# Optimization experiments

Measured on AMD Instinct MI355X. Metric: run time of the kernel, lower is better.

Reference implementation:

```python
import jax, jax.numpy as jnp
import numpy as np

N_LOC, N_EVT, E = 100000, 200000, 1000000
F_LOC, F_EVT, H = 128, 128, 64


def setup_inputs() -> dict:
    key = jax.random.key(0)
    ks = jax.random.split(key, 12)
    s = lambda k, shp: jax.random.normal(k, shp, dtype=jnp.float32) * (1.0 / np.sqrt(shp[0]))
    return {
        "loc_x": jax.random.normal(ks[0], (N_LOC, F_LOC), dtype=jnp.float32),
        "evt_x": jax.random.normal(ks[1], (N_EVT, F_EVT), dtype=jnp.float32),
        "edge_index": jax.random.randint(ks[2], (2, E), 0, N_LOC, dtype=jnp.int64),
        # projections (stored as (in, out))
        "W_loc": s(ks[3], (F_LOC, H)), "b_loc": jnp.zeros((H,), jnp.float32),
        "W_evt": s(ks[4], (F_EVT, H)), "b_evt": jnp.zeros((H,), jnp.float32),
        # SAGEConv: lin_l (on aggregated src, with bias), lin_r (on dst root, no bias)
        "W_l": s(ks[5], (H, H)), "b_l": jnp.zeros((H,), jnp.float32),
        "W_r": s(ks[6], (H, H)),
        # head MLP
        "W_h1": s(ks[7], (H, H // 2)), "b_h1": jnp.zeros((H // 2,), jnp.float32),
        "W_h2": s(ks[8], (H // 2, 1)), "b_h2": jnp.zeros((1,), jnp.float32),
    }


def reference(loc_x, evt_x, edge_index, W_loc, b_loc, W_evt, b_evt,
              W_l, b_l, W_r, W_h1, b_h1, W_h2, b_h2):
    # node projections + ReLU
    loc_h = jax.nn.relu(loc_x @ W_loc + b_loc)   # [N_loc, H]
    evt_h = jax.nn.relu(evt_x @ W_evt + b_evt)   # [N_evt, H]

    src, dst = edge_index[0], edge_index[1]      # event -> location
    n_loc = loc_h.shape[0]
    # mean aggregation of source (event) features onto destination (location) nodes
    msg_sum = jax.ops.segment_sum(evt_h[src], dst, num_segments=n_loc)   # [N_loc, H]
    cnt = jax.ops.segment_sum(jnp.ones_like(dst, dtype=loc_h.dtype), dst,
                              num_segments=n_loc)
    agg = msg_sum / jnp.maximum(cnt, 1.0)[:, None]
    # SAGEConv: lin_l(agg) + lin_r(root), then ReLU
    loc_h = jax.nn.relu(agg @ W_l + b_l + loc_h @ W_r)

    # prediction head
    h = jax.nn.relu(loc_h @ W_h1 + b_h1)
    logits = (h @ W_h2 + b_h2)[:, 0]             # [N_loc]
    return logits
```

## Files before the change

### kernel.cpp

```cpp
#include <hip/hip_runtime.h>


#define N_LOC 100000
#define N_EVT 200000
#define E_CNT 1000000
#define NTILES 6250
#define NBKT   256
#define BKT_L  391
#define CAPG   6000
#define QCAP   32
#define BKT_BLK 512
#define PERB   1954

#define PROJ_EVT_BLK 1536
#define PROJ_LOC_BLK 768
#define PROJ_BLK_TOT (PROJ_EVT_BLK + PROJ_LOC_BLK)
#define EVT_TILES 12500
#define LOC_TILES 6250
#define HEAD_BLK  1024

typedef __attribute__((ext_vector_type(8))) short short8;
typedef __attribute__((ext_vector_type(4))) float floatx4;
typedef __attribute__((ext_vector_type(8))) unsigned short ushort8v;

__device__ __forceinline__ float b2f(unsigned short u) {
    unsigned int x = ((unsigned int)u) << 16;
    return __builtin_bit_cast(float, x);
}
__device__ __forceinline__ unsigned short f2b(float f) {
    unsigned int x = __builtin_bit_cast(unsigned int, f);
    unsigned int r = (x + 0x7fffu + ((x >> 16) & 1u)) >> 16;
    return (unsigned short)r;
}
__device__ __forceinline__ float loadf(const void* p, int f32, size_t i) {
    return f32 ? ((const float*)p)[i] : b2f(((const unsigned short*)p)[i]);
}

__global__ __launch_bounds__(256) void prep_kernel(
    const void* t0, const void* t1, const int* eidx,
    const void* t3, const void* t4, const void* t5, const void* t6,
    const void* t7, const void* t8, const void* t9, const void* t10,
    const void* t11, const void* t12, const void* t13,
    int* flags, int* gbc, unsigned short* __restrict__ wp_all) {
    int b = blockIdx.x, tid = threadIdx.x;
    __shared__ int s0, s1;

    if (b == 14) { gbc[tid] = 0; return; }

    if (b >= 15) {
        int pb = b - 15;
        const void* W; int K, N, bstart, off;
        if (pb < 4)       { W = t5;  K = 128; N = 64; bstart = 0;  off = 0; }
        else if (pb < 8)  { W = t3;  K = 128; N = 64; bstart = 4;  off = 8192; }
        else if (pb < 10) { W = t7;  K = 64;  N = 64; bstart = 8;  off = 16384; }
        else if (pb < 12) { W = t9;  K = 64;  N = 64; bstart = 10; off = 20480; }
        else              { W = t10; K = 64;  N = 32; bstart = 12; off = 24576; }
        if (tid == 0) s0 = 0;
        __syncthreads();
        int nsamp = 2 * K * N; if (nsamp > 1024) nsamp = 1024;
        const unsigned short* h = (const unsigned short*)W;
        int susp = 0;
        for (int i = tid; i < nsamp; i += 256)
            if (((h[i] >> 7) & 0xFF) >= 0x90) susp++;
        if (susp) atomicAdd(&s0, susp);
        __syncthreads();
        int f32 = (s0 * 16 >= nsamp) ? 1 : 0;

        int idx  = (pb - bstart) * 256 + tid;
        int nk   = K >> 5;
        int f    = idx >> 6;
        int lane = idx & 63;
        int t  = f / nk;
        int kk = f - t * nk;
        int n  = t * 16 + (lane & 15);
        int k0 = kk * 32 + (lane >> 4) * 8;
        unsigned short tmp[8];
#pragma unroll
        for (int j = 0; j < 8; ++j) {
            size_t src = (size_t)(k0 + j) * N + n;
            tmp[j] = f32 ? f2b(((const float*)W)[src])
                         : ((const unsigned short*)W)[src];
        }
#pragma unroll
        for (int j = 0; j < 8; ++j) wp_all[(size_t)off + (size_t)idx * 8 + j] = tmp[j];
        return;
    }

    if (tid == 0) { s0 = 0; s1 = 0; }
    __syncthreads();
    if (b == 13) {
        if (tid < 128) {
            if (eidx[2 * tid] != 0) atomicAdd(&s0, 1);
            if (eidx[2 * tid + 1] != 0) atomicAdd(&s1, 1);
        }
        __syncthreads();
        if (tid == 0) flags[2] = (s1 == 0 && s0 > 32) ? 1 : 0;
        return;
    }
    const void* ptrs[13] = {t0, t1, t3, t4, t5, t6, t7, t8, t9, t10, t11, t12, t13};
    const int   cnts[13] = {12800000, 25600000, 8192, 64, 8192, 64,
                            4096, 64, 4096, 2048, 32, 32, 1};
    const int   slot[13] = {0, 1, 3, 4, 5, 6, 7, 8, 9, 10, 11, 12, 13};
    int nsamp = 2 * cnts[b];
    if (nsamp > 1024) nsamp = 1024;
    const unsigned short* h = (const unsigned short*)ptrs[b];
    int susp = 0;
    for (int i = tid; i < nsamp; i += 256)
        if (((h[i] >> 7) & 0xFF) >= 0x90) susp++;
    if (susp) atomicAdd(&s0, susp);
    __syncthreads();
    if (tid == 0) flags[slot[b]] = (s0 * 16 >= nsamp) ? 1 : 0;
}

__global__ __launch_bounds__(256, 3) void proj_both_kernel(
    const void* __restrict__ evt_x, const void* __restrict__ loc_x,
    const unsigned short* __restrict__ wp_all,
    const void* __restrict__ b_evt, const void* __restrict__ b_loc,
    unsigned short* __restrict__ evt_h, unsigned short* __restrict__ loc_h,
    const int* __restrict__ flags) {
    __shared__ unsigned short bs[8192];
    int blk = blockIdx.x;
    int tid = threadIdx.x, lane = tid & 63, wv = tid >> 6;
    int l15 = lane & 15, quad = lane >> 4;

    const void* X; const unsigned short* Wp; const void* bias;
    unsigned short* Y; int fx, fb, w0, nw, ntile;
    if (blk < PROJ_EVT_BLK) {
        X = evt_x; Wp = wp_all;        bias = b_evt; Y = evt_h;
        fx = flags[1]; fb = flags[6];
        w0 = blk * 4 + wv; nw = PROJ_EVT_BLK * 4; ntile = EVT_TILES;
    } else {
        X = loc_x; Wp = wp_all + 8192; bias = b_loc; Y = loc_h;
        fx = flags[0]; fb = flags[4];
        w0 = (blk - PROJ_EVT_BLK) * 4 + wv; nw = PROJ_LOC_BLK * 4; ntile = LOC_TILES;
    }

    {
        const short8* src = reinterpret_cast<const short8*>(Wp);
        short8* dst = reinterpret_cast<short8*>(bs);
#pragma unroll
        for (int i = 0; i < 4; ++i) dst[tid + i * 256] = src[tid + i * 256];
    }
    __syncthreads();

    float bv[4];
#pragma unroll
    for (int q = 0; q < 4; ++q) bv[q] = loadf(bias, fb, q * 16 + l15);

    if (w0 >= ntile) return;

    auto mfma_store = [&](const short8* a, int t) {
        floatx4 acc[4];
#pragma unroll
        for (int q = 0; q < 4; ++q) acc[q] = (floatx4)0.0f;
#pragma unroll
        for (int q = 0; q < 4; ++q) {
            short8 bq[4];
#pragma unroll
            for (int kk = 0; kk < 4; ++kk)
                bq[kk] = *reinterpret_cast<const short8*>(
                    &bs[((q * 4 + kk) * 64 + lane) * 8]);
#pragma unroll
            for (int kk = 0; kk < 4; ++kk)
                acc[q] = __builtin_amdgcn_mfma_f32_16x16x32_bf16(
                    a[kk], bq[kk], acc[q], 0, 0, 0);
        }
#pragma unroll
        for (int q = 0; q < 4; ++q)
#pragma unroll
            for (int r = 0; r < 4; ++r) {
                float v = acc[q][r] + bv[q];
                v = v > 0.0f ? v : 0.0f;
                Y[(size_t)(t * 16 + quad * 4 + r) * 64 + q * 16 + l15] = f2b(v);
            }
    };

    if (fx) {
        const float* Xf = (const float*)X;
        float4 pf[8];
        auto issueF = [&](int t) {
            const float* xr = Xf + (size_t)(t * 16 + l15) * 128 + quad * 8;
#pragma unroll
            for (int kk = 0; kk < 4; ++kk) {
                pf[kk * 2]     = *reinterpret_cast<const float4*>(xr + kk * 32);
                pf[kk * 2 + 1] = *reinterpret_cast<const float4*>(xr + kk * 32 + 4);
            }
        };
        issueF(w0);
        for (int t = w0; t < ntile; t += nw) {
            short8 a[4];
#pragma unroll
            for (int kk = 0; kk < 4; ++kk) {
                float4 p0 = pf[kk * 2], p1 = pf[kk * 2 + 1];
                short8 v;
                v[0] = (short)f2b(p0.x); v[1] = (short)f2b(p0.y);
                v[2] = (short)f2b(p0.z); v[3] = (short)f2b(p0.w);
                v[4] = (short)f2b(p1.x); v[5] = (short)f2b(p1.y);
                v[6] = (short)f2b(p1.z); v[7] = (short)f2b(p1.w);
                a[kk] = v;
            }
            int tn = t + nw;
            if (tn < ntile) issueF(tn);
            mfma_store(a, t);
        }
    } else {
        const unsigned short* Xh = (const unsigned short*)X;
        short8 an[4];
        auto issueH = [&](int t) {
            const unsigned short* xr = Xh + (size_t)(t * 16 + l15) * 128 + quad * 8;
#pragma unroll
            for (int kk = 0; kk < 4; ++kk)
                an[kk] = *reinterpret_cast<const short8*>(xr + kk * 32);
        };
        issueH(w0);
        for (int t = w0; t < ntile; t += nw) {
            short8 a[4];
#pragma unroll
            for (int kk = 0; kk < 4; ++kk) a[kk] = an[kk];
            int tn = t + nw;
            if (tn < ntile) issueH(tn);
            mfma_store(a, t);
        }
    }
}

__global__ __launch_bounds__(256) void bucket_kernel(
    const int* __restrict__ eidx, uint2* __restrict__ bkt,
    int* __restrict__ gbc, const int* __restrict__ flags) {
    __shared__ uint2 queue[NBKT][QCAP];
    __shared__ int qcnt[NBKT];
    int tid = threadIdx.x, blk = blockIdx.x;
    qcnt[tid] = 0;
    __syncthreads();
    int f64 = flags[2];
    const long long* e64 = (const long long*)eidx;
    int e0 = blk * PERB;
    int e1 = e0 + PERB; if (e1 > E_CNT) e1 = E_CNT;
    const int rounds = (PERB + 255) / 256;

    for (int r = 0; r < rounds; ++r) {
        int e = e0 + r * 256 + tid;
        if (e < e1) {
            int src, dst;
            if (f64) { src = (int)e64[e]; dst = (int)e64[E_CNT + e]; }
            else     { src = eidx[e];     dst = eidx[E_CNT + e]; }
            if ((unsigned)dst < (unsigned)N_LOC && (unsigned)src < (unsigned)N_EVT) {
                int bk = dst / BKT_L;
                int pos = atomicAdd(&qcnt[bk], 1);
                if (pos < QCAP) {
                    queue[bk][pos] = make_uint2((unsigned)src, (unsigned)dst);
                } else {
                    int p = atomicAdd(&gbc[bk], 1);
                    if (p < CAPG) bkt[(size_t)bk * CAPG + p] = make_uint2(src, dst);
                }
            }
        }
        __syncthreads();
        int n = qcnt[tid]; if (n > QCAP) n = QCAP;
        while (n >= 16) {
            int gp = atomicAdd(&gbc[tid], 16);
            if (gp + 16 <= CAPG) {
                uint2* d = bkt + (size_t)tid * CAPG + gp;
#pragma unroll
                for (int j = 0; j < 16; ++j) d[j] = queue[tid][j];
            }
#pragma unroll
            for (int j = 16; j < QCAP; ++j) queue[tid][j - 16] = queue[tid][j];
            n -= 16;
        }
        qcnt[tid] = n;
        __syncthreads();
    }
    int n = qcnt[tid]; if (n > QCAP) n = QCAP;
    if (n > 0) {
        int gp = atomicAdd(&gbc[tid], n);
        for (int j = 0; j < n; ++j)
            if (gp + j < CAPG) bkt[(size_t)tid * CAPG + gp + j] = queue[tid][j];
    }
}

__global__ __launch_bounds__(256) void csr_build_kernel(
    const uint2* __restrict__ bkt, const int* __restrict__ gbc,
    int* __restrict__ rowptr, int* __restrict__ csr) {
    __shared__ int sg[256];
    __shared__ int lcnt[512];
    __shared__ int lscan[512];
    __shared__ int lcsr[CAPG];
    int b = blockIdx.x, tid = threadIdx.x;
    int loc0 = b * BKT_L;
    int nloc = N_LOC - loc0; if (nloc > BKT_L) nloc = BKT_L;

    int gv = gbc[tid]; if (gv > CAPG) gv = CAPG;
    sg[tid] = gv;
    __syncthreads();
    for (int d = 1; d < 256; d <<= 1) {
        int x = (tid >= d) ? sg[tid - d] : 0;
        __syncthreads();
        sg[tid] += x;
        __syncthreads();
    }
    int cntE = gbc[b]; if (cntE > CAPG) cntE = CAPG;
    int base = sg[b] - cntE;
    const uint2* bp = bkt + (size_t)b * CAPG;

    int i0 = tid, i1 = tid + 256;
    lcnt[i0] = 0; lcnt[i1] = 0;
    __syncthreads();
    for (int i = tid; i < cntE; i += 256) {
        int d = (int)bp[i].y - loc0;
        atomicAdd(&lcnt[d], 1);
    }
    __syncthreads();
    lscan[i0] = lcnt[i0]; lscan[i1] = lcnt[i1];
    __syncthreads();
    for (int d = 1; d < 512; d <<= 1) {
        int v0 = (i0 >= d) ? lscan[i0 - d] : 0;
        int v1 = (i1 >= d) ? lscan[i1 - d] : 0;
        __syncthreads();
        lscan[i0] += v0; lscan[i1] += v1;
        __syncthreads();
    }
    for (int i = tid; i < nloc; i += 256) {
        int excl = lscan[i] - lcnt[i];
        rowptr[loc0 + i] = base + excl;
        lcnt[i] = excl;
    }
    if (b == NBKT - 1 && tid == 0) rowptr[N_LOC] = base + cntE;
    __syncthreads();
    for (int i = tid; i < cntE; i += 256) {
        uint2 pr = bp[i];
        int d = (int)pr.y - loc0;
        int p = atomicAdd(&lcnt[d], 1);
        if (p < CAPG) lcsr[p] = (int)pr.x;
    }
    __syncthreads();
    for (int i = tid; i < cntE; i += 256) csr[base + i] = lcsr[i];
}

__global__ __launch_bounds__(256) void aggregate_kernel(
    const unsigned short* __restrict__ evt_h,
    const int* __restrict__ rowptr, const int* __restrict__ csr,
    unsigned short* __restrict__ agg, int N) {
    int wid  = (blockIdx.x * 256 + threadIdx.x) >> 6;
    int lane = threadIdx.x & 63;
    int eo = lane >> 3, cg = lane & 7;
    if (wid >= N) return;
    int e0 = rowptr[wid], e1 = rowptr[wid + 1];
    float a[8];
#pragma unroll
    for (int k = 0; k < 8; ++k) a[k] = 0.0f;

    int j = e0;
    for (; j + 16 <= e1; j += 16) {
        int s0 = csr[j + eo];
        int s1 = csr[j + 8 + eo];
        ushort8v v0 = *reinterpret_cast<const ushort8v*>(
            evt_h + (size_t)s0 * 64 + cg * 8);
        ushort8v v1 = *reinterpret_cast<const ushort8v*>(
            evt_h + (size_t)s1 * 64 + cg * 8);
#pragma unroll
        for (int k = 0; k < 8; ++k) a[k] += b2f(v0[k]) + b2f(v1[k]);
    }
    for (; j < e1; j += 8) {
        int jj = j + eo;
        bool c = jj < e1;
        int s = csr[c ? jj : j];
        ushort8v v = *reinterpret_cast<const ushort8v*>(
            evt_h + (size_t)s * 64 + cg * 8);
        if (c) {
#pragma unroll
            for (int k = 0; k < 8; ++k) a[k] += b2f(v[k]);
        }
    }
#pragma unroll
    for (int k = 0; k < 8; ++k) {
        a[k] += __shfl_xor(a[k], 8);
        a[k] += __shfl_xor(a[k], 16);
        a[k] += __shfl_xor(a[k], 32);
    }
    float inv = (e1 > e0) ? 1.0f / (float)(e1 - e0) : 0.0f;
    if (eo == 0) {
        ushort8v o;
#pragma unroll
        for (int k = 0; k < 8; ++k) o[k] = f2b(a[k] * inv);
        *reinterpret_cast<ushort8v*>(agg + (size_t)wid * 64 + cg * 8) = o;
    }
}

__global__ __launch_bounds__(256, 3) void head_kernel(
    const unsigned short* __restrict__ agg,
    const unsigned short* __restrict__ loc_h,
    const unsigned short* __restrict__ wp_all,
    const void* __restrict__ bl, const void* __restrict__ bh1,
    const void* __restrict__ wh2, const void* __restrict__ bh2,
    void* __restrict__ out, const int* __restrict__ flags) {
    __shared__ unsigned short bls[4096];
    __shared__ unsigned short brs[4096];
    __shared__ unsigned short b1s[2048];
    __shared__ unsigned short h2s[4][16 * 64];
    int tid = threadIdx.x, lane = tid & 63, wv = tid >> 6;
    int l15 = lane & 15, quad = lane >> 4;
    int fbl = flags[8], fbh1 = flags[11], fwh2 = flags[12], fbh2 = flags[13];
    int fout = flags[0];
    const unsigned short* wp_l  = wp_all + 16384;
    const unsigned short* wp_r  = wp_all + 20480;
    const unsigned short* wp_h1 = wp_all + 24576;

    {
        const short8* sl = reinterpret_cast<const short8*>(wp_l);
        const short8* sr = reinterpret_cast<const short8*>(wp_r);
        const short8* s1 = reinterpret_cast<const short8*>(wp_h1);
        short8* dl = reinterpret_cast<short8*>(bls);
        short8* dr = reinterpret_cast<short8*>(brs);
        short8* d1 = reinterpret_cast<short8*>(b1s);
        dl[tid] = sl[tid]; dl[tid + 256] = sl[tid + 256];
        dr[tid] = sr[tid]; dr[tid + 256] = sr[tid + 256];
        d1[tid] = s1[tid];
    }
    __syncthreads();

    float bbl[4], bh1v[2], w2v[2];
#pragma unroll
    for (int q = 0; q < 4; ++q) bbl[q] = loadf(bl, fbl, q * 16 + l15);
#pragma unroll
    for (int q = 0; q < 2; ++q) {
        bh1v[q] = loadf(bh1, fbh1, q * 16 + l15);
        w2v[q]  = loadf(wh2, fwh2, q * 16 + l15);
    }
    float bb2 = loadf(bh2, fbh2, 0);

    const int NW = HEAD_BLK * 4;
    int w0 = blockIdx.x * 4 + wv;
    if (w0 >= NTILES) return;

    short8 c0[4], c1[4];

    auto issue = [&](short8* c, int t) {
        int m = t * 16 + l15;
#pragma unroll
        for (int kk = 0; kk < 2; ++kk) {
            c[kk]     = *reinterpret_cast<const short8*>(
                agg + (size_t)m * 64 + kk * 32 + quad * 8);
            c[2 + kk] = *reinterpret_cast<const short8*>(
                loc_h + (size_t)m * 64 + kk * 32 + quad * 8);
        }
    };

    auto compute = [&](const short8* c, int tile) {
        floatx4 acc[4];
#pragma unroll
        for (int q = 0; q < 4; ++q) acc[q] = (floatx4)0.0f;
#pragma unroll
        for (int q = 0; q < 4; ++q) {
            short8 bwl[2], bwr[2];
#pragma unroll
            for (int kk = 0; kk < 2; ++kk) {
                bwl[kk] = *reinterpret_cast<const short8*>(
                    &bls[((q * 2 + kk) * 64 + lane) * 8]);
                bwr[kk] = *reinterpret_cast<const short8*>(
                    &brs[((q * 2 + kk) * 64 + lane) * 8]);
            }
#pragma unroll
            for (int kk = 0; kk < 2; ++kk) {
                acc[q] = __builtin_amdgcn_mfma_f32_16x16x32_bf16(
                    c[kk], bwl[kk], acc[q], 0, 0, 0);
                acc[q] = __builtin_amdgcn_mfma_f32_16x16x32_bf16(
                    c[2 + kk], bwr[kk], acc[q], 0, 0, 0);
            }
        }
#pragma unroll
        for (int q = 0; q < 4; ++q)
#pragma unroll
            for (int r = 0; r < 4; ++r) {
                float v = acc[q][r] + bbl[q];
                v = v > 0.0f ? v : 0.0f;
                h2s[wv][(quad * 4 + r) * 64 + q * 16 + l15] = f2b(v);
            }
        short8 aH[2];
#pragma unroll
        for (int kk = 0; kk < 2; ++kk)
            aH[kk] = *reinterpret_cast<const short8*>(
                &h2s[wv][l15 * 64 + kk * 32 + quad * 8]);

        floatx4 a1[2];
#pragma unroll
        for (int q = 0; q < 2; ++q) a1[q] = (floatx4)0.0f;
#pragma unroll
        for (int q = 0; q < 2; ++q) {
            short8 bw1[2];
#pragma unroll
            for (int kk = 0; kk < 2; ++kk)
                bw1[kk] = *reinterpret_cast<const short8*>(
                    &b1s[((q * 2 + kk) * 64 + lane) * 8]);
#pragma unroll
            for (int kk = 0; kk < 2; ++kk)
                a1[q] = __builtin_amdgcn_mfma_f32_16x16x32_bf16(
                    aH[kk], bw1[kk], a1[q], 0, 0, 0);
        }

        float s[4] = {0.f, 0.f, 0.f, 0.f};
#pragma unroll
        for (int q = 0; q < 2; ++q)
#pragma unroll
            for (int r = 0; r < 4; ++r) {
                float v = a1[q][r] + bh1v[q];
                v = v > 0.0f ? v : 0.0f;
                s[r] += v * w2v[q];
            }
#pragma unroll
        for (int r = 0; r < 4; ++r) {
            s[r] += __shfl_xor(s[r], 1);
            s[r] += __shfl_xor(s[r], 2);
            s[r] += __shfl_xor(s[r], 4);
            s[r] += __shfl_xor(s[r], 8);
        }
#pragma unroll
        for (int r = 0; r < 4; ++r) {
            if (l15 == r) {
                int row = tile * 16 + quad * 4 + r;
                float v = s[r] + bb2;
                if (fout) ((float*)out)[row] = v;
                else      ((unsigned short*)out)[row] = f2b(v);
            }
        }
    };

    issue(c0, w0);
    int t = w0;
    while (true) {
        int tn = t + NW;
        bool hn = tn < NTILES;
        if (hn) issue(c1, tn);
        compute(c0, t);
        if (!hn) break;
        t = tn; tn = t + NW; hn = tn < NTILES;
        if (hn) issue(c0, tn);
        compute(c1, t);
        if (!hn) break;
        t = tn;
    }
}

extern "C" void kernel_launch(void* const* d_in, const int* in_sizes, int n_in,
                              void* d_out, int out_size, void* d_ws, size_t ws_size,
                              hipStream_t stream) {
    (void)in_sizes; (void)n_in; (void)out_size; (void)ws_size;
    const void* loc_x = d_in[0];
    const void* evt_x = d_in[1];
    const int*  eidx  = (const int*)d_in[2];
    const void* W_loc = d_in[3];
    const void* b_loc = d_in[4];
    const void* W_evt = d_in[5];
    const void* b_evt = d_in[6];
    const void* W_l   = d_in[7];
    const void* b_l   = d_in[8];
    const void* W_r   = d_in[9];
    const void* W_h1  = d_in[10];
    const void* b_h1  = d_in[11];
    const void* W_h2  = d_in[12];
    const void* b_h2  = d_in[13];

    char* ws = (char*)d_ws;
    unsigned short* evt_h  = (unsigned short*)(ws);
    unsigned short* loc_h  = (unsigned short*)(ws + 25600000);
    int*            csr    = (int*)(ws + 38400000);
    int*            rowptr = (int*)(ws + 42400000);
    int*            gbc    = (int*)(ws + 42800016);
    unsigned short* wp_all = (unsigned short*)(ws + 42802064);
    int*            flags  = (int*)(ws + 42855312);
    uint2*          bkt    = (uint2*)(ws + 42855376);
    unsigned short* agg    = (unsigned short*)(ws + 42855376);

    prep_kernel<<<28, 256, 0, stream>>>(
        loc_x, evt_x, eidx, W_loc, b_loc, W_evt, b_evt,
        W_l, b_l, W_r, W_h1, b_h1, W_h2, b_h2,
        flags, gbc, wp_all);

    proj_both_kernel<<<PROJ_BLK_TOT, 256, 0, stream>>>(
        evt_x, loc_x, wp_all, b_evt, b_loc, evt_h, loc_h, flags);

    bucket_kernel<<<BKT_BLK, 256, 0, stream>>>(eidx, bkt, gbc, flags);
    csr_build_kernel<<<NBKT, 256, 0, stream>>>(bkt, gbc, rowptr, csr);

    aggregate_kernel<<<(N_LOC + 3) / 4, 256, 0, stream>>>(evt_h, rowptr, csr,
                                                          agg, N_LOC);

    head_kernel<<<HEAD_BLK, 256, 0, stream>>>(
        agg, loc_h, wp_all, b_l, b_h1, W_h2, b_h2, d_out, flags);
}
```

Baseline: 300.6 us.

## Fuse mean aggregation into head kernel via per-wave LDS tile

Merges the separate aggregate and head kernels into one kernel. Each wave aggregates 16 destination rows sequentially into a padded LDS tile, then runs the SAGE linear layers and the MLP head on that tile with MFMA. This removes the global write and re-read of the aggregated features and one launch. The cost is that each wave now processes 16 rows serially, giving less memory-level parallelism during the gather, and the software prefetch pipeline over tiles is dropped.

```diff
diff --git a/kernel.cpp b/kernel.cpp
--- a/kernel.cpp
+++ b/kernel.cpp
@@ -17,7 +17,7 @@
 #define PROJ_BLK_TOT (PROJ_EVT_BLK + PROJ_LOC_BLK)
 #define EVT_TILES 12500
 #define LOC_TILES 6250
-#define HEAD_BLK  1024
+#define AGGH_BLK  1563
 
 typedef __attribute__((ext_vector_type(8))) short short8;
 typedef __attribute__((ext_vector_type(4))) float floatx4;
@@ -337,59 +337,10 @@
     for (int i = tid; i < cntE; i += 256) csr[base + i] = lcsr[i];
 }
 
-__global__ __launch_bounds__(256) void aggregate_kernel(
+__global__ __launch_bounds__(256, 3) void agg_head_kernel(
     const unsigned short* __restrict__ evt_h,
+    const unsigned short* __restrict__ loc_h,
     const int* __restrict__ rowptr, const int* __restrict__ csr,
-    unsigned short* __restrict__ agg, int N) {
-    int wid  = (blockIdx.x * 256 + threadIdx.x) >> 6;
-    int lane = threadIdx.x & 63;
-    int eo = lane >> 3, cg = lane & 7;
-    if (wid >= N) return;
-    int e0 = rowptr[wid], e1 = rowptr[wid + 1];
-    float a[8];
-#pragma unroll
-    for (int k = 0; k < 8; ++k) a[k] = 0.0f;
-
-    int j = e0;
-    for (; j + 16 <= e1; j += 16) {
-        int s0 = csr[j + eo];
-        int s1 = csr[j + 8 + eo];
-        ushort8v v0 = *reinterpret_cast<const ushort8v*>(
-            evt_h + (size_t)s0 * 64 + cg * 8);
-        ushort8v v1 = *reinterpret_cast<const ushort8v*>(
-            evt_h + (size_t)s1 * 64 + cg * 8);
-#pragma unroll
-        for (int k = 0; k < 8; ++k) a[k] += b2f(v0[k]) + b2f(v1[k]);
-    }
-    for (; j < e1; j += 8) {
-        int jj = j + eo;
-        bool c = jj < e1;
-        int s = csr[c ? jj : j];
-        ushort8v v = *reinterpret_cast<const ushort8v*>(
-            evt_h + (size_t)s * 64 + cg * 8);
-        if (c) {
-#pragma unroll
-            for (int k = 0; k < 8; ++k) a[k] += b2f(v[k]);
-        }
-    }
-#pragma unroll
-    for (int k = 0; k < 8; ++k) {
-        a[k] += __shfl_xor(a[k], 8);
-        a[k] += __shfl_xor(a[k], 16);
-        a[k] += __shfl_xor(a[k], 32);
-    }
-    float inv = (e1 > e0) ? 1.0f / (float)(e1 - e0) : 0.0f;
-    if (eo == 0) {
-        ushort8v o;
-#pragma unroll
-        for (int k = 0; k < 8; ++k) o[k] = f2b(a[k] * inv);
-        *reinterpret_cast<ushort8v*>(agg + (size_t)wid * 64 + cg * 8) = o;
-    }
-}
-
-__global__ __launch_bounds__(256, 3) void head_kernel(
-    const unsigned short* __restrict__ agg,
-    const unsigned short* __restrict__ loc_h,
     const unsigned short* __restrict__ wp_all,
     const void* __restrict__ bl, const void* __restrict__ bh1,
     const void* __restrict__ wh2, const void* __restrict__ bh2,
@@ -398,6 +349,7 @@
     __shared__ unsigned short brs[4096];
     __shared__ unsigned short b1s[2048];
     __shared__ unsigned short h2s[4][16 * 64];
+    __shared__ unsigned short ag[4][16 * 72];
     int tid = threadIdx.x, lane = tid & 63, wv = tid >> 6;
     int l15 = lane & 15, quad = lane >> 4;
     int fbl = flags[8], fbh1 = flags[11], fwh2 = flags[12], fbh2 = flags[13];
@@ -429,115 +381,143 @@
     }
     float bb2 = loadf(bh2, fbh2, 0);
 
-    const int NW = HEAD_BLK * 4;
-    int w0 = blockIdx.x * 4 + wv;
-    if (w0 >= NTILES) return;
-
-    short8 c0[4], c1[4];
-
-    auto issue = [&](short8* c, int t) {
-        int m = t * 16 + l15;
+    int tile = blockIdx.x * 4 + wv;
+    if (tile >= NTILES) return;
+
+    short8 cl[2];
+#pragma unroll
+    for (int kk = 0; kk < 2; ++kk)
+        cl[kk] = *reinterpret_cast<const short8*>(
+            loc_h + (size_t)(tile * 16 + l15) * 64 + kk * 32 + quad * 8);
+
+    unsigned short* arow = &ag[wv][0];
+    int eo = lane >> 3, cg = lane & 7;
+    for (int r = 0; r < 16; ++r) {
+        int row = tile * 16 + r;
+        int e0 = rowptr[row], e1 = rowptr[row + 1];
+        float a[8];
+#pragma unroll
+        for (int k = 0; k < 8; ++k) a[k] = 0.0f;
+        int j = e0;
+        for (; j + 16 <= e1; j += 16) {
+            int s0 = csr[j + eo];
+            int s1 = csr[j + 8 + eo];
+            ushort8v v0 = *reinterpret_cast<const ushort8v*>(
+                evt_h + (size_t)s0 * 64 + cg * 8);
+            ushort8v v1 = *reinterpret_cast<const ushort8v*>(
+                evt_h + (size_t)s1 * 64 + cg * 8);
+#pragma unroll
+            for (int k = 0; k < 8; ++k) a[k] += b2f(v0[k]) + b2f(v1[k]);
+        }
+        for (; j < e1; j += 8) {
+            int jj = j + eo;
+            bool c = jj < e1;
+            int s = csr[c ? jj : j];
+            ushort8v v = *reinterpret_cast<const ushort8v*>(
+                evt_h + (size_t)s * 64 + cg * 8);
+            if (c) {
+#pragma unroll
+                for (int k = 0; k < 8; ++k) a[k] += b2f(v[k]);
+            }
+        }
+#pragma unroll
+        for (int k = 0; k < 8; ++k) {
+            a[k] += __shfl_xor(a[k], 8);
+            a[k] += __shfl_xor(a[k], 16);
+            a[k] += __shfl_xor(a[k], 32);
+        }
+        float inv = (e1 > e0) ? 1.0f / (float)(e1 - e0) : 0.0f;
+        if (eo == 0) {
+            ushort8v o;
+#pragma unroll
+            for (int k = 0; k < 8; ++k) o[k] = f2b(a[k] * inv);
+            *reinterpret_cast<ushort8v*>(arow + r * 72 + cg * 8) = o;
+        }
+    }
+
+    short8 c[4];
+#pragma unroll
+    for (int kk = 0; kk < 2; ++kk) {
+        c[kk] = *reinterpret_cast<const short8*>(
+            arow + l15 * 72 + kk * 32 + quad * 8);
+        c[2 + kk] = cl[kk];
+    }
+
+    floatx4 acc[4];
+#pragma unroll
+    for (int q = 0; q < 4; ++q) acc[q] = (floatx4)0.0f;
+#pragma unroll
+    for (int q = 0; q < 4; ++q) {
+        short8 bwl[2], bwr[2];
 #pragma unroll
         for (int kk = 0; kk < 2; ++kk) {
-            c[kk]     = *reinterpret_cast<const short8*>(
-                agg + (size_t)m * 64 + kk * 32 + quad * 8);
-            c[2 + kk] = *reinterpret_cast<const short8*>(
-                loc_h + (size_t)m * 64 + kk * 32 + quad * 8);
-        }
-    };
-
-    auto compute = [&](const short8* c, int tile) {
-        floatx4 acc[4];
-#pragma unroll
-        for (int q = 0; q < 4; ++q) acc[q] = (floatx4)0.0f;
-#pragma unroll
-        for (int q = 0; q < 4; ++q) {
-            short8 bwl[2], bwr[2];
-#pragma unroll
-            for (int kk = 0; kk < 2; ++kk) {
-                bwl[kk] = *reinterpret_cast<const short8*>(
-                    &bls[((q * 2 + kk) * 64 + lane) * 8]);
-                bwr[kk] = *reinterpret_cast<const short8*>(
-                    &brs[((q * 2 + kk) * 64 + lane) * 8]);
-            }
-#pragma unroll
-            for (int kk = 0; kk < 2; ++kk) {
-                acc[q] = __builtin_amdgcn_mfma_f32_16x16x32_bf16(
-                    c[kk], bwl[kk], acc[q], 0, 0, 0);
-                acc[q] = __builtin_amdgcn_mfma_f32_16x16x32_bf16(
-                    c[2 + kk], bwr[kk], acc[q], 0, 0, 0);
-            }
-        }
-#pragma unroll
-        for (int q = 0; q < 4; ++q)
-#pragma unroll
-            for (int r = 0; r < 4; ++r) {
-                float v = acc[q][r] + bbl[q];
-                v = v > 0.0f ? v : 0.0f;
-                h2s[wv][(quad * 4 + r) * 64 + q * 16 + l15] = f2b(v);
-            }
-        short8 aH[2];
+            bwl[kk] = *reinterpret_cast<const short8*>(
+                &bls[((q * 2 + kk) * 64 + lane) * 8]);
+            bwr[kk] = *reinterpret_cast<const short8*>(
+                &brs[((q * 2 + kk) * 64 + lane) * 8]);
+        }
+#pragma unroll
+        for (int kk = 0; kk < 2; ++kk) {
+            acc[q] = __builtin_amdgcn_mfma_f32_16x16x32_bf16(
+                c[kk], bwl[kk], acc[q], 0, 0, 0);
+            acc[q] = __builtin_amdgcn_mfma_f32_16x16x32_bf16(
+                c[2 + kk], bwr[kk], acc[q], 0, 0, 0);
+        }
+    }
+#pragma unroll
+    for (int q = 0; q < 4; ++q)
+#pragma unroll
+        for (int r = 0; r < 4; ++r) {
+            float v = acc[q][r] + bbl[q];
+            v = v > 0.0f ? v : 0.0f;
+            h2s[wv][(quad * 4 + r) * 64 + q * 16 + l15] = f2b(v);
+        }
+    short8 aH[2];
+#pragma unroll
+    for (int kk = 0; kk < 2; ++kk)
+        aH[kk] = *reinterpret_cast<const short8*>(
+            &h2s[wv][l15 * 64 + kk * 32 + quad * 8]);
+
+    floatx4 a1[2];
+#pragma unroll
+    for (int q = 0; q < 2; ++q) a1[q] = (floatx4)0.0f;
+#pragma unroll
+    for (int q = 0; q < 2; ++q) {
+        short8 bw1[2];
 #pragma unroll
         for (int kk = 0; kk < 2; ++kk)
-            aH[kk] = *reinterpret_cast<const short8*>(
-                &h2s[wv][l15 * 64 + kk * 32 + quad * 8]);
-
-        floatx4 a1[2];
-#pragma unroll
-        for (int q = 0; q < 2; ++q) a1[q] = (floatx4)0.0f;
-#pragma unroll
-        for (int q = 0; q < 2; ++q) {
-            short8 bw1[2];
-#pragma unroll
-            for (int kk = 0; kk < 2; ++kk)
-                bw1[kk] = *reinterpret_cast<const short8*>(
-                    &b1s[((q * 2 + kk) * 64 + lane) * 8]);
-#pragma unroll
-            for (int kk = 0; kk < 2; ++kk)
-                a1[q] = __builtin_amdgcn_mfma_f32_16x16x32_bf16(
-                    aH[kk], bw1[kk], a1[q], 0, 0, 0);
-        }
-
-        float s[4] = {0.f, 0.f, 0.f, 0.f};
-#pragma unroll
-        for (int q = 0; q < 2; ++q)
-#pragma unroll
-            for (int r = 0; r < 4; ++r) {
-                float v = a1[q][r] + bh1v[q];
-                v = v > 0.0f ? v : 0.0f;
-                s[r] += v * w2v[q];
-            }
+            bw1[kk] = *reinterpret_cast<const short8*>(
+                &b1s[((q * 2 + kk) * 64 + lane) * 8]);
+#pragma unroll
+        for (int kk = 0; kk < 2; ++kk)
+            a1[q] = __builtin_amdgcn_mfma_f32_16x16x32_bf16(
+                aH[kk], bw1[kk], a1[q], 0, 0, 0);
+    }
+
+    float s[4] = {0.f, 0.f, 0.f, 0.f};
+#pragma unroll
+    for (int q = 0; q < 2; ++q)
 #pragma unroll
         for (int r = 0; r < 4; ++r) {
-            s[r] += __shfl_xor(s[r], 1);
-            s[r] += __shfl_xor(s[r], 2);
-            s[r] += __shfl_xor(s[r], 4);
-            s[r] += __shfl_xor(s[r], 8);
-        }
-#pragma unroll
-        for (int r = 0; r < 4; ++r) {
-            if (l15 == r) {
-                int row = tile * 16 + quad * 4 + r;
-                float v = s[r] + bb2;
-                if (fout) ((float*)out)[row] = v;
-                else      ((unsigned short*)out)[row] = f2b(v);
-            }
-        }
-    };
-
-    issue(c0, w0);
-    int t = w0;
-    while (true) {
-        int tn = t + NW;
-        bool hn = tn < NTILES;
-        if (hn) issue(c1, tn);
-        compute(c0, t);
-        if (!hn) break;
-        t = tn; tn = t + NW; hn = tn < NTILES;
-        if (hn) issue(c0, tn);
-        compute(c1, t);
-        if (!hn) break;
-        t = tn;
+            float v = a1[q][r] + bh1v[q];
+            v = v > 0.0f ? v : 0.0f;
+            s[r] += v * w2v[q];
+        }
+#pragma unroll
+    for (int r = 0; r < 4; ++r) {
+        s[r] += __shfl_xor(s[r], 1);
+        s[r] += __shfl_xor(s[r], 2);
+        s[r] += __shfl_xor(s[r], 4);
+        s[r] += __shfl_xor(s[r], 8);
+    }
+#pragma unroll
+    for (int r = 0; r < 4; ++r) {
+        if (l15 == r) {
+            int row = tile * 16 + quad * 4 + r;
+            float v = s[r] + bb2;
+            if (fout) ((float*)out)[row] = v;
+            else      ((unsigned short*)out)[row] = f2b(v);
+        }
     }
 }
 
@@ -569,7 +549,6 @@
     unsigned short* wp_all = (unsigned short*)(ws + 42802064);
     int*            flags  = (int*)(ws + 42855312);
     uint2*          bkt    = (uint2*)(ws + 42855376);
-    unsigned short* agg    = (unsigned short*)(ws + 42855376);
 
     prep_kernel<<<28, 256, 0, stream>>>(
         loc_x, evt_x, eidx, W_loc, b_loc, W_evt, b_evt,
@@ -582,9 +561,7 @@
     bucket_kernel<<<BKT_BLK, 256, 0, stream>>>(eidx, bkt, gbc, flags);
     csr_build_kernel<<<NBKT, 256, 0, stream>>>(bkt, gbc, rowptr, csr);
 
-    aggregate_kernel<<<(N_LOC + 3) / 4, 256, 0, stream>>>(evt_h, rowptr, csr,
-                                                          agg, N_LOC);
-
-    head_kernel<<<HEAD_BLK, 256, 0, stream>>>(
-        agg, loc_h, wp_all, b_l, b_h1, W_h2, b_h2, d_out, flags);
-}
+    agg_head_kernel<<<AGGH_BLK, 256, 0, stream>>>(
+        evt_h, loc_h, rowptr, csr, wp_all,
+        b_l, b_h1, W_h2, b_h2, d_out, flags);
+}
```

Measured after the change: 329.0 us. +9.5%, slower.
